# Kernel optimization log

Measured on AMD Instinct MI355X. Metric: run time of the kernel, lower is better.

## Reference

```python
import jax, jax.numpy as jnp
import numpy as np

H, DI, N, R, B, L, K = 1024, 2048, 16, 64, 1, 2048, 4


def setup_inputs() -> dict:
    key = jax.random.key(0)
    ks = jax.random.split(key, 12)
    s = 0.02
    x = jax.random.normal(ks[0], (B, L, H), dtype=jnp.float32)
    in_proj_w = jax.random.normal(ks[1], (2 * DI, H), dtype=jnp.float32) * s
    in_proj_b = jax.random.normal(ks[2], (2 * DI,), dtype=jnp.float32) * s
    conv_w = jax.random.normal(ks[3], (DI, 1, K), dtype=jnp.float32) * s
    conv_b = jax.random.normal(ks[4], (DI,), dtype=jnp.float32) * s
    x_proj_w = jax.random.normal(ks[5], (R + 2 * N, DI), dtype=jnp.float32) * s
    dt_init_std = R ** (-0.5)
    dt_proj_w = jax.random.uniform(ks[6], (DI, R), dtype=jnp.float32, minval=-dt_init_std, maxval=dt_init_std)
    dt = jnp.exp(jax.random.uniform(ks[7], (DI,), dtype=jnp.float32) * (np.log(0.1) - np.log(0.001)) + np.log(0.001))
    dt = jnp.clip(dt, 0.0001, None)
    dt_proj_b = dt + jnp.log(-jnp.expm1(-dt))
    A_log = jnp.log(jnp.broadcast_to(jnp.arange(1, N + 1, dtype=jnp.float32)[None, :], (DI, N)))
    D = jnp.ones((DI,), dtype=jnp.float32)
    out_proj_w = jax.random.normal(ks[8], (H, DI), dtype=jnp.float32) * s
    return {"x": x, "in_proj_w": in_proj_w, "in_proj_b": in_proj_b, "conv_w": conv_w,
            "conv_b": conv_b, "x_proj_w": x_proj_w, "dt_proj_w": dt_proj_w,
            "dt_proj_b": dt_proj_b, "A_log": A_log, "D": D, "out_proj_w": out_proj_w}


def _mamba_fwd(x, in_proj_w, in_proj_b, conv_w, conv_b, x_proj_w, dt_proj_w, dt_proj_b, A_log, D, out_proj_w):
    b, l, _ = x.shape
    x_and_res = x @ in_proj_w.T + in_proj_b               # [b, l, 2*DI]
    xc, res = jnp.split(x_and_res, 2, axis=-1)
    # causal depthwise conv1d (padding K-1 then truncate to l == left-pad only)
    xt = jnp.transpose(xc, (0, 2, 1))                     # [b, DI, l]
    conv = jax.lax.conv_general_dilated(
        xt, conv_w, window_strides=(1,), padding=[(K - 1, 0)],
        dimension_numbers=("NCH", "OIH", "NCH"), feature_group_count=DI)
    conv = conv + conv_b[None, :, None]
    xs = jnp.transpose(jax.nn.silu(conv), (0, 2, 1))      # [b, l, DI]
    # SSM
    A = -jnp.exp(A_log.astype(jnp.float32))               # [DI, N]
    x_dbl = xs @ x_proj_w.T                               # [b, l, R+2N]
    delta, Bm, Cm = jnp.split(x_dbl, [R, R + N], axis=-1)
    delta = jax.nn.softplus(delta @ dt_proj_w.T + dt_proj_b)   # [b, l, DI]
    deltaA = jnp.exp(delta[..., None] * A[None, None])         # [b, l, DI, N]
    deltaB_u = delta[..., None] * Bm[:, :, None, :] * xs[..., None]

    def comb(c1, c2):
        a1, u1 = c1
        a2, u2 = c2
        return a2 * a1, a2 * u1 + u2

    _, h = jax.lax.associative_scan(comb, (deltaA, deltaB_u), axis=1)
    y = jnp.einsum("bldn,bln->bld", h, Cm) + xs * D.astype(jnp.float32)
    y = y * jax.nn.silu(res)
    return y @ out_proj_w.T                               # [b, l, H]


def reference(x, in_proj_w, in_proj_b, conv_w, conv_b, x_proj_w, dt_proj_w, dt_proj_b, A_log, D, out_proj_w):
    return _mamba_fwd(x, in_proj_w, in_proj_b, conv_w, conv_b, x_proj_w,
                      dt_proj_w, dt_proj_b, A_log, D, out_proj_w)
```

## Files before the change

kernel.cpp:

```cpp
#include <hip/hip_runtime.h>
#include <hip/hip_bf16.h>
#include <math.h>

#define H_DIM 1024
#define DI    2048
#define NS    16
#define RR    64
#define LL    2048
#define NC    64
#define CL    32
#define KSPL  16

typedef __bf16 bf16x8 __attribute__((ext_vector_type(8)));
typedef __bf16 bf16x4 __attribute__((ext_vector_type(4)));
typedef float  f32x4  __attribute__((ext_vector_type(4)));

__device__ __forceinline__ float silu_f(float x)  { return x / (1.f + __expf(-x)); }
__device__ __forceinline__ float softplus_f(float x) {
    const float l = __logf(1.f + __expf(x));
    return x > 15.f ? x : l;
}

__device__ __forceinline__ void gload16(const void* g, void* l) {
    __builtin_amdgcn_global_load_lds(
        (const __attribute__((address_space(1))) void*)g,
        (__attribute__((address_space(3))) void*)l, 16, 0, 0);
}

__device__ __forceinline__ void f2b4(const float* __restrict__ in,
                                     __bf16* __restrict__ out)
{
    float4 v = *(const float4*)in;
    bf16x4 o;
    o[0] = (__bf16)v.x; o[1] = (__bf16)v.y; o[2] = (__bf16)v.z; o[3] = (__bf16)v.w;
    *(bf16x4*)out = o;
}

__device__ __forceinline__ void xcd_swz(int nx, int ny, int& bx, int& by)
{
    const int nwg = nx * ny;
    const int bid = by * nx + bx;
    const int cpx = nwg >> 3;
    const int s   = (bid & 7) * cpx + (bid >> 3);
    bx = s % nx;  by = s / nx;
}

#define SEG0 (LL * H_DIM)
#define SEG1 (2 * DI * H_DIM)
#define SEG2 (H_DIM * DI)
#define SEG3 (DI * RR)
#define SEG4 (128 * DI)
#define CUM0 SEG0
#define CUM1 (CUM0 + SEG1)
#define CUM2 (CUM1 + SEG2)
#define CUM3 (CUM2 + SEG3)
#define CUMT (CUM3 + SEG4)

__global__ __launch_bounds__(256) void convert_all_k(
    const float* __restrict__ x,    const float* __restrict__ in_w,
    const float* __restrict__ outw, const float* __restrict__ dtw,
    const float* __restrict__ xpw,
    __bf16* __restrict__ x_bf,    __bf16* __restrict__ inw_bf,
    __bf16* __restrict__ outw_bf, __bf16* __restrict__ dtw_bf,
    __bf16* __restrict__ xpw_pad)
{
    const int i = (blockIdx.x * 256 + threadIdx.x) * 4;
    if (i < CUM0) {
        f2b4(x + i, x_bf + i);
    } else if (i < CUM1) {
        const int o = i - CUM0;  f2b4(in_w + o, inw_bf + o);
    } else if (i < CUM2) {
        const int o = i - CUM1;  f2b4(outw + o, outw_bf + o);
    } else if (i < CUM3) {
        const int o = i - CUM2;  f2b4(dtw + o, dtw_bf + o);
    } else if (i < CUMT) {
        const int o = i - CUM3;
        const int row = o >> 11;
        if (row < 96) {
            f2b4(xpw + o, xpw_pad + o);
        } else {
            bf16x4 z; z[0] = z[1] = z[2] = z[3] = (__bf16)0.f;
            *(bf16x4*)&xpw_pad[o] = z;
        }
    }
}

__global__ __launch_bounds__(256) void reduce_xdbl_k(
    const float* __restrict__ part, float* __restrict__ xdbl,
    __bf16* __restrict__ xdbl_bf)
{
    const int idx = blockIdx.x * 256 + threadIdx.x;
    float s = 0.f;
    #pragma unroll
    for (int z = 0; z < KSPL; ++z) s += part[(size_t)z * (LL * 96) + idx];
    xdbl[idx] = s;
    xdbl_bf[idx] = (__bf16)s;
}

__global__ __launch_bounds__(256) void reduce_out_k(
    const float* __restrict__ part, float* __restrict__ out)
{
    const int i = (blockIdx.x * 256 + threadIdx.x) * 4;
    f32x4 a = *(const f32x4*)&part[i];
    f32x4 b = *(const f32x4*)&part[(size_t)LL * H_DIM + i];
    *(f32x4*)&out[i] = a + b;
}

#define WAIT_VM3()  asm volatile("s_waitcnt vmcnt(3)" ::: "memory")
#define WAIT_VM0()  asm volatile("s_waitcnt vmcnt(0)" ::: "memory")

__global__ __launch_bounds__(256) void gemm_inproj_k(
    const __bf16* __restrict__ A,
    const __bf16* __restrict__ W,
    const float* __restrict__ bias,
    __bf16* __restrict__ xc_bf,
    __bf16* __restrict__ res_bf)
{
    __shared__ __bf16 smA[3][64 * 32];
    __shared__ __bf16 smB[3][128 * 32];
    const int t    = threadIdx.x;
    const int lane = t & 63;
    int bx = blockIdx.x, by = blockIdx.y;
    xcd_swz(32, 32, bx, by);
    const int m0 = by * 64, n0 = bx * 128;
    const int wr = ((t >> 6) >> 1) * 32;
    const int wc = ((t >> 6) & 1) * 64;

    const int srow = t >> 2;
    const int skof = (t & 3) * 8;
    const int lds_base = (t >> 6) * 512;

    const int offA = (wr + (lane & 15)) * 32 + ((lane >> 4) * 8);
    const int offB = (wc + (lane & 15)) * 32 + ((lane >> 4) * 8);

    f32x4 acc[2][4] = {};

#define STAGE_IP(buf, k0)                                                          \
    do {                                                                           \
        gload16(A + (size_t)(m0 + srow)      * H_DIM + (k0) + skof, &smA[buf][lds_base]);        \
        gload16(W + (size_t)(n0 + srow)      * H_DIM + (k0) + skof, &smB[buf][lds_base]);        \
        gload16(W + (size_t)(n0 + 64 + srow) * H_DIM + (k0) + skof, &smB[buf][2048 + lds_base]); \
    } while (0)

    const int nk = H_DIM / 32;
    STAGE_IP(0, 0);
    STAGE_IP(1, 32);
    for (int ks = 0; ks < nk; ++ks) {
        if (ks + 1 < nk) WAIT_VM3(); else WAIT_VM0();
        __builtin_amdgcn_s_barrier();
        if (ks + 2 < nk) STAGE_IP((ks + 2) % 3, (ks + 2) * 32);
        const int cb = ks % 3;

        bf16x8 af[2], bfr[4];
        #pragma unroll
        for (int m = 0; m < 2; ++m) af[m]  = *(const bf16x8*)&smA[cb][offA + m * 512];
        #pragma unroll
        for (int n = 0; n < 4; ++n) bfr[n] = *(const bf16x8*)&smB[cb][offB + n * 512];
        #pragma unroll
        for (int m = 0; m < 2; ++m)
            #pragma unroll
            for (int n = 0; n < 4; ++n)
                acc[m][n] = __builtin_amdgcn_mfma_f32_16x16x32_bf16(
                    af[m], bfr[n], acc[m][n], 0, 0, 0);
    }
#undef STAGE_IP

    __bf16* outp = (n0 < DI) ? xc_bf : res_bf;
    const int ncol0 = (n0 < DI) ? n0 : n0 - DI;
    const int rbase = m0 + wr + ((lane >> 4) << 2);
    const int cbase = ncol0 + wc + (lane & 15);
    #pragma unroll
    for (int n = 0; n < 4; ++n) {
        const int col = cbase + n * 16;
        const float bv = bias[(n0 < DI ? 0 : DI) + col];
        #pragma unroll
        for (int m = 0; m < 2; ++m)
            #pragma unroll
            for (int j = 0; j < 4; ++j)
                outp[(size_t)(rbase + m * 16 + j) * DI + col] =
                    (__bf16)(acc[m][n][j] + bv);
    }
}

template<int BIAS, int ACT, int SPLITK, int SWZ>
__global__ __launch_bounds__(256) void gemm64_bf16_nt(
    const __bf16* __restrict__ A, int lda,
    const __bf16* __restrict__ W, int ldw,
    const float* __restrict__ bias,
    float* __restrict__ C, int ldc, int ncols, size_t pstride,
    int K)
{
    __shared__ __bf16 smA[3][64 * 32];
    __shared__ __bf16 smB[3][128 * 32];
    const int t    = threadIdx.x;
    const int lane = t & 63;
    int bx = blockIdx.x, by = blockIdx.y;
    if (SWZ) xcd_swz(gridDim.x, gridDim.y, bx, by);
    const int m0 = by * 64, n0 = bx * 128;
    const int wr = ((t >> 6) >> 1) * 32;
    const int wc = ((t >> 6) & 1) * 64;

    const int srow = t >> 2;
    const int skof = (t & 3) * 8;
    const int lds_base = (t >> 6) * 512;

    const int offA = (wr + (lane & 15)) * 32 + ((lane >> 4) * 8);
    const int offB = (wc + (lane & 15)) * 32 + ((lane >> 4) * 8);

    const int kseg  = K / SPLITK;
    const int kbase = (SPLITK > 1) ? blockIdx.z * kseg : 0;

    f32x4 acc[2][4] = {};

#define STAGE_64(buf, k0)                                                          \
    do {                                                                           \
        gload16(A + (size_t)(m0 + srow)      * lda + (k0) + skof, &smA[buf][lds_base]);        \
        gload16(W + (size_t)(n0 + srow)      * ldw + (k0) + skof, &smB[buf][lds_base]);        \
        gload16(W + (size_t)(n0 + 64 + srow) * ldw + (k0) + skof, &smB[buf][2048 + lds_base]); \
    } while (0)

    const int nk = kseg / 32;
    STAGE_64(0, kbase);
    if (nk > 1) STAGE_64(1, kbase + 32);
    for (int ks = 0; ks < nk; ++ks) {
        if (ks + 1 < nk) WAIT_VM3(); else WAIT_VM0();
        __builtin_amdgcn_s_barrier();
        if (ks + 2 < nk) STAGE_64((ks + 2) % 3, kbase + (ks + 2) * 32);
        const int cb = ks % 3;

        bf16x8 af[2], bfr[4];
        #pragma unroll
        for (int m = 0; m < 2; ++m) af[m]  = *(const bf16x8*)&smA[cb][offA + m * 512];
        #pragma unroll
        for (int n = 0; n < 4; ++n) bfr[n] = *(const bf16x8*)&smB[cb][offB + n * 512];
        #pragma unroll
        for (int m = 0; m < 2; ++m)
            #pragma unroll
            for (int n = 0; n < 4; ++n)
                acc[m][n] = __builtin_amdgcn_mfma_f32_16x16x32_bf16(
                    af[m], bfr[n], acc[m][n], 0, 0, 0);
    }
#undef STAGE_64

    float* Cp = C + ((SPLITK > 1) ? (size_t)blockIdx.z * pstride : 0);
    const int rbase = m0 + wr + ((lane >> 4) << 2);
    const int cbase = n0 + wc + (lane & 15);
    #pragma unroll
    for (int n = 0; n < 4; ++n) {
        const int col = cbase + n * 16;
        if (col >= ncols) continue;
        const float bv = BIAS ? bias[col] : 0.f;
        #pragma unroll
        for (int m = 0; m < 2; ++m) {
            #pragma unroll
            for (int j = 0; j < 4; ++j) {
                float v = acc[m][n][j] + bv;
                if (ACT == 1) v = softplus_f(v);
                Cp[(size_t)(rbase + m * 16 + j) * ldc + col] = v;
            }
        }
    }
}

__global__ __launch_bounds__(256) void conv_silu_k(
    const __bf16* __restrict__ xc, const float* __restrict__ cw,
    const float* __restrict__ cb, __bf16* __restrict__ xs_bf)
{
    const int idx = blockIdx.x * 256 + threadIdx.x;
    const int l  = idx >> 8;
    const int d0 = (idx & 255) * 8;

    float r0[8] = {}, r1[8] = {}, r2[8] = {}, r3[8];
    bf16x8 v;
    if (l >= 3) { v = *(const bf16x8*)&xc[(size_t)(l-3)*DI + d0];
                  #pragma unroll
                  for (int j = 0; j < 8; ++j) r0[j] = (float)v[j]; }
    if (l >= 2) { v = *(const bf16x8*)&xc[(size_t)(l-2)*DI + d0];
                  #pragma unroll
                  for (int j = 0; j < 8; ++j) r1[j] = (float)v[j]; }
    if (l >= 1) { v = *(const bf16x8*)&xc[(size_t)(l-1)*DI + d0];
                  #pragma unroll
                  for (int j = 0; j < 8; ++j) r2[j] = (float)v[j]; }
    v = *(const bf16x8*)&xc[(size_t)l*DI + d0];
    #pragma unroll
    for (int j = 0; j < 8; ++j) r3[j] = (float)v[j];

    bf16x8 o;
    #pragma unroll
    for (int j = 0; j < 8; ++j) {
        const int d = d0 + j;
        float4 w = *(const float4*)&cw[d * 4];
        float a = cb[d];
        a = fmaf(r0[j], w.x, a);
        a = fmaf(r1[j], w.y, a);
        a = fmaf(r2[j], w.z, a);
        a = fmaf(r3[j], w.w, a);
        o[j] = (__bf16)silu_f(a);
    }
    *(bf16x8*)&xs_bf[(size_t)l*DI + d0] = o;
}

__global__ __launch_bounds__(256) void scan1_k(
    const float* __restrict__ delta, const __bf16* __restrict__ xs,
    const float* __restrict__ A_log, const float* __restrict__ xdbl,
    float* __restrict__ P, float* __restrict__ S)
{
    const int d = blockIdx.x * 256 + threadIdx.x;
    const int c = blockIdx.y;
    float A[NS];
    #pragma unroll
    for (int n = 0; n < NS; ++n) A[n] = -__expf(A_log[d * NS + n]);
    float h[NS] = {};
    float ap[NS];
    #pragma unroll
    for (int n = 0; n < NS; ++n) ap[n] = 1.f;

    const int l0 = c * CL;
    for (int l = l0; l < l0 + CL; ++l) {
        const float dt = delta[(size_t)l * DI + d];
        const float u  = (float)xs[(size_t)l * DI + d];
        const float du = dt * u;
        #pragma unroll
        for (int n = 0; n < NS; ++n) {
            const float Bn = xdbl[(size_t)l * 96 + RR + n];
            const float dA = __expf(dt * A[n]);
            h[n]  = fmaf(dA, h[n], du * Bn);
            ap[n] *= dA;
        }
    }
    const size_t base = ((size_t)c * DI + d) * NS;
    #pragma unroll
    for (int n = 0; n < NS; ++n) { P[base + n] = ap[n]; S[base + n] = h[n]; }
}

__global__ __launch_bounds__(256) void scan2_k(
    const float* __restrict__ P, const float* __restrict__ S, float* __restrict__ Hp)
{
    const int idx = blockIdx.x * 256 + threadIdx.x;
    float h = 0.f;
    for (int c = 0; c < NC; ++c) {
        const size_t o = (size_t)c * DI * NS + idx;
        Hp[o] = h;
        h = fmaf(P[o], h, S[o]);
    }
}

__global__ __launch_bounds__(256) void scan3_k(
    const float* __restrict__ delta, const __bf16* __restrict__ xs,
    const float* __restrict__ A_log, const float* __restrict__ xdbl,
    const float* __restrict__ Hp, const __bf16* __restrict__ res_bf,
    const float* __restrict__ Dp, __bf16* __restrict__ y_bf)
{
    const int d = blockIdx.x * 256 + threadIdx.x;
    const int c = blockIdx.y;
    float A[NS];
    #pragma unroll
    for (int n = 0; n < NS; ++n) A[n] = -__expf(A_log[d * NS + n]);
    float h[NS];
    const size_t base = ((size_t)c * DI + d) * NS;
    #pragma unroll
    for (int n = 0; n < NS; ++n) h[n] = Hp[base + n];
    const float Dd = Dp[d];

    const int l0 = c * CL;
    for (int l = l0; l < l0 + CL; ++l) {
        const float dt = delta[(size_t)l * DI + d];
        const float u  = (float)xs[(size_t)l * DI + d];
        const float du = dt * u;
        float acc = 0.f;
        #pragma unroll
        for (int n = 0; n < NS; ++n) {
            const float Bn = xdbl[(size_t)l * 96 + RR + n];
            const float Cn = xdbl[(size_t)l * 96 + RR + NS + n];
            const float dA = __expf(dt * A[n]);
            h[n] = fmaf(dA, h[n], du * Bn);
            acc  = fmaf(h[n], Cn, acc);
        }
        float yv = fmaf(u, Dd, acc);
        const float r = (float)res_bf[(size_t)l * DI + d];
        yv *= silu_f(r);
        y_bf[(size_t)l * DI + d] = (__bf16)yv;
    }
}

extern "C" void kernel_launch(void* const* d_in, const int* in_sizes, int n_in,
                              void* d_out, int out_size, void* d_ws, size_t ws_size,
                              hipStream_t stream)
{
    const float* x        = (const float*)d_in[0];
    const float* in_w     = (const float*)d_in[1];
    const float* in_b     = (const float*)d_in[2];
    const float* conv_w   = (const float*)d_in[3];
    const float* conv_b   = (const float*)d_in[4];
    const float* xproj_w  = (const float*)d_in[5];
    const float* dtproj_w = (const float*)d_in[6];
    const float* dtproj_b = (const float*)d_in[7];
    const float* A_log    = (const float*)d_in[8];
    const float* Dp       = (const float*)d_in[9];
    const float* outw     = (const float*)d_in[10];
    float* out = (float*)d_out;

    float* ws    = (float*)d_ws;
    float* delta = ws;
    float* xdbl  = delta + (size_t)LL * DI;
    float* P     = xdbl  + (size_t)LL * 96;
    float* S     = P     + (size_t)NC * DI * NS;
    float* Hp    = S     + (size_t)NC * DI * NS;
    float* opart = Hp    + (size_t)NC * DI * NS;
    float* xpart = delta;
    __bf16* x_bf    = (__bf16*)(opart + (size_t)2 * LL * H_DIM);
    __bf16* inw_bf  = x_bf    + (size_t)LL * H_DIM;
    __bf16* outw_bf = inw_bf  + (size_t)2 * DI * H_DIM;
    __bf16* dtw_bf  = outw_bf + (size_t)H_DIM * DI;
    __bf16* xdbl_bf = dtw_bf  + (size_t)DI * RR;
    __bf16* y_bf    = xdbl_bf + (size_t)LL * 96;
    __bf16* xs_bf   = y_bf    + (size_t)LL * DI;
    __bf16* xc_bf   = xs_bf   + (size_t)LL * DI;
    __bf16* res_bf  = xc_bf   + (size_t)LL * DI;
    __bf16* xpw_pad = res_bf  + (size_t)LL * DI;

    const dim3 blk(256);

    convert_all_k<<<dim3(CUMT / 1024), blk, 0, stream>>>(
        x, in_w, outw, dtproj_w, xproj_w,
        x_bf, inw_bf, outw_bf, dtw_bf, xpw_pad);

    gemm_inproj_k<<<dim3((2*DI)/128, LL/64), blk, 0, stream>>>(
        x_bf, inw_bf, in_b, xc_bf, res_bf);

    conv_silu_k<<<dim3((LL*DI)/(8*256)), blk, 0, stream>>>(xc_bf, conv_w, conv_b, xs_bf);

    gemm64_bf16_nt<0,0,KSPL,0><<<dim3(1, LL/64, KSPL), blk, 0, stream>>>(
        xs_bf, DI, xpw_pad, DI, nullptr, xpart, 96, 96, (size_t)LL * 96, DI);
    reduce_xdbl_k<<<dim3((LL * 96) / 256), blk, 0, stream>>>(xpart, xdbl, xdbl_bf);

    gemm64_bf16_nt<1,1,1,1><<<dim3(DI/128, LL/64), blk, 0, stream>>>(
        xdbl_bf, 96, dtw_bf, RR, dtproj_b, delta, DI, DI, 0, RR);

    scan1_k<<<dim3(DI/256, NC), blk, 0, stream>>>(delta, xs_bf, A_log, xdbl, P, S);
    scan2_k<<<dim3((DI*NS)/256), blk, 0, stream>>>(P, S, Hp);
    scan3_k<<<dim3(DI/256, NC), blk, 0, stream>>>(delta, xs_bf, A_log, xdbl, Hp, res_bf, Dp, y_bf);

    gemm64_bf16_nt<0,0,2,1><<<dim3(H_DIM/128, LL/64, 2), blk, 0, stream>>>(
        y_bf, DI, outw_bf, DI, nullptr, opart, H_DIM, H_DIM, (size_t)LL * H_DIM, DI);
    reduce_out_k<<<dim3((LL * H_DIM) / 1024), blk, 0, stream>>>(opart, out);
}
```

Measured before the change: 243.7 us.

## Switch GEMMs to 32-row tiles and drop split-K on out_proj

Replaces the 64x128 triple-buffered GEMM with a 32x128 tile, double-buffered variant using __syncthreads between stages, with each wave owning a 32-column slice. The out_proj GEMM now runs without split-K and writes directly to the output, removing the partial buffer and the reduce kernel. The smaller M tile doubles the block count to keep occupancy up without split-K. In exchange, each block does half as much work per loaded B tile, and the loop drops from three buffers to two with a full barrier every step, which gives less load/compute overlap.

```diff
diff --git a/kernel.cpp b/kernel.cpp
--- a/kernel.cpp
+++ b/kernel.cpp
@@ -97,15 +97,6 @@
     xdbl_bf[idx] = (__bf16)s;
 }
 
-__global__ __launch_bounds__(256) void reduce_out_k(
-    const float* __restrict__ part, float* __restrict__ out)
-{
-    const int i = (blockIdx.x * 256 + threadIdx.x) * 4;
-    f32x4 a = *(const f32x4*)&part[i];
-    f32x4 b = *(const f32x4*)&part[(size_t)LL * H_DIM + i];
-    *(f32x4*)&out[i] = a + b;
-}
-
 #define WAIT_VM3()  asm volatile("s_waitcnt vmcnt(3)" ::: "memory")
 #define WAIT_VM0()  asm volatile("s_waitcnt vmcnt(0)" ::: "memory")
 
@@ -183,70 +174,70 @@
 }
 
 template<int BIAS, int ACT, int SPLITK, int SWZ>
-__global__ __launch_bounds__(256) void gemm64_bf16_nt(
+__global__ __launch_bounds__(256) void gemm32_bf16_nt(
     const __bf16* __restrict__ A, int lda,
     const __bf16* __restrict__ W, int ldw,
     const float* __restrict__ bias,
     float* __restrict__ C, int ldc, int ncols, size_t pstride,
     int K)
 {
-    __shared__ __bf16 smA[3][64 * 32];
-    __shared__ __bf16 smB[3][128 * 32];
+    __shared__ __bf16 smA[2][32 * 32];
+    __shared__ __bf16 smB[2][128 * 32];
     const int t    = threadIdx.x;
     const int lane = t & 63;
+    const int wv   = t >> 6;
     int bx = blockIdx.x, by = blockIdx.y;
     if (SWZ) xcd_swz(gridDim.x, gridDim.y, bx, by);
-    const int m0 = by * 64, n0 = bx * 128;
-    const int wr = ((t >> 6) >> 1) * 32;
-    const int wc = ((t >> 6) & 1) * 64;
+    const int m0 = by * 32, n0 = bx * 128;
 
     const int srow = t >> 2;
     const int skof = (t & 3) * 8;
-    const int lds_base = (t >> 6) * 512;
-
-    const int offA = (wr + (lane & 15)) * 32 + ((lane >> 4) * 8);
-    const int offB = (wc + (lane & 15)) * 32 + ((lane >> 4) * 8);
+    const int lds_base = wv * 512;
+
+    const int offA = (lane & 15) * 32 + ((lane >> 4) * 8);
+    const int offB = (wv * 32 + (lane & 15)) * 32 + ((lane >> 4) * 8);
 
     const int kseg  = K / SPLITK;
     const int kbase = (SPLITK > 1) ? blockIdx.z * kseg : 0;
-
-    f32x4 acc[2][4] = {};
-
-#define STAGE_64(buf, k0)                                                          \
+    const int kend  = kbase + kseg;
+
+    f32x4 acc[2][2] = {};
+
+#define STAGE_32(buf, k0)                                                          \
     do {                                                                           \
-        gload16(A + (size_t)(m0 + srow)      * lda + (k0) + skof, &smA[buf][lds_base]);        \
+        if (t < 128)                                                               \
+            gload16(A + (size_t)(m0 + srow)  * lda + (k0) + skof, &smA[buf][lds_base]);        \
         gload16(W + (size_t)(n0 + srow)      * ldw + (k0) + skof, &smB[buf][lds_base]);        \
         gload16(W + (size_t)(n0 + 64 + srow) * ldw + (k0) + skof, &smB[buf][2048 + lds_base]); \
     } while (0)
 
-    const int nk = kseg / 32;
-    STAGE_64(0, kbase);
-    if (nk > 1) STAGE_64(1, kbase + 32);
-    for (int ks = 0; ks < nk; ++ks) {
-        if (ks + 1 < nk) WAIT_VM3(); else WAIT_VM0();
-        __builtin_amdgcn_s_barrier();
-        if (ks + 2 < nk) STAGE_64((ks + 2) % 3, kbase + (ks + 2) * 32);
-        const int cb = ks % 3;
-
-        bf16x8 af[2], bfr[4];
-        #pragma unroll
-        for (int m = 0; m < 2; ++m) af[m]  = *(const bf16x8*)&smA[cb][offA + m * 512];
-        #pragma unroll
-        for (int n = 0; n < 4; ++n) bfr[n] = *(const bf16x8*)&smB[cb][offB + n * 512];
+    STAGE_32(0, kbase);
+    __syncthreads();
+    int cur = 0;
+    for (int k0 = kbase; k0 < kend; k0 += 32) {
+        if (k0 + 32 < kend) STAGE_32(cur ^ 1, k0 + 32);
+
+        bf16x8 af[2], bfr[2];
+        #pragma unroll
+        for (int m = 0; m < 2; ++m) af[m]  = *(const bf16x8*)&smA[cur][offA + m * 512];
+        #pragma unroll
+        for (int n = 0; n < 2; ++n) bfr[n] = *(const bf16x8*)&smB[cur][offB + n * 512];
         #pragma unroll
         for (int m = 0; m < 2; ++m)
             #pragma unroll
-            for (int n = 0; n < 4; ++n)
+            for (int n = 0; n < 2; ++n)
                 acc[m][n] = __builtin_amdgcn_mfma_f32_16x16x32_bf16(
                     af[m], bfr[n], acc[m][n], 0, 0, 0);
-    }
-#undef STAGE_64
+        __syncthreads();
+        cur ^= 1;
+    }
+#undef STAGE_32
 
     float* Cp = C + ((SPLITK > 1) ? (size_t)blockIdx.z * pstride : 0);
-    const int rbase = m0 + wr + ((lane >> 4) << 2);
-    const int cbase = n0 + wc + (lane & 15);
-    #pragma unroll
-    for (int n = 0; n < 4; ++n) {
+    const int rbase = m0 + ((lane >> 4) << 2);
+    const int cbase = n0 + wv * 32 + (lane & 15);
+    #pragma unroll
+    for (int n = 0; n < 2; ++n) {
         const int col = cbase + n * 16;
         if (col >= ncols) continue;
         const float bv = BIAS ? bias[col] : 0.f;
@@ -406,9 +397,8 @@
     float* P     = xdbl  + (size_t)LL * 96;
     float* S     = P     + (size_t)NC * DI * NS;
     float* Hp    = S     + (size_t)NC * DI * NS;
-    float* opart = Hp    + (size_t)NC * DI * NS;
     float* xpart = delta;
-    __bf16* x_bf    = (__bf16*)(opart + (size_t)2 * LL * H_DIM);
+    __bf16* x_bf    = (__bf16*)(Hp + (size_t)NC * DI * NS);
     __bf16* inw_bf  = x_bf    + (size_t)LL * H_DIM;
     __bf16* outw_bf = inw_bf  + (size_t)2 * DI * H_DIM;
     __bf16* dtw_bf  = outw_bf + (size_t)H_DIM * DI;
@@ -430,18 +420,17 @@
 
     conv_silu_k<<<dim3((LL*DI)/(8*256)), blk, 0, stream>>>(xc_bf, conv_w, conv_b, xs_bf);
 
-    gemm64_bf16_nt<0,0,KSPL,0><<<dim3(1, LL/64, KSPL), blk, 0, stream>>>(
+    gemm32_bf16_nt<0,0,KSPL,0><<<dim3(1, LL/32, KSPL), blk, 0, stream>>>(
         xs_bf, DI, xpw_pad, DI, nullptr, xpart, 96, 96, (size_t)LL * 96, DI);
     reduce_xdbl_k<<<dim3((LL * 96) / 256), blk, 0, stream>>>(xpart, xdbl, xdbl_bf);
 
-    gemm64_bf16_nt<1,1,1,1><<<dim3(DI/128, LL/64), blk, 0, stream>>>(
+    gemm32_bf16_nt<1,1,1,1><<<dim3(DI/128, LL/32), blk, 0, stream>>>(
         xdbl_bf, 96, dtw_bf, RR, dtproj_b, delta, DI, DI, 0, RR);
 
     scan1_k<<<dim3(DI/256, NC), blk, 0, stream>>>(delta, xs_bf, A_log, xdbl, P, S);
     scan2_k<<<dim3((DI*NS)/256), blk, 0, stream>>>(P, S, Hp);
     scan3_k<<<dim3(DI/256, NC), blk, 0, stream>>>(delta, xs_bf, A_log, xdbl, Hp, res_bf, Dp, y_bf);
 
-    gemm64_bf16_nt<0,0,2,1><<<dim3(H_DIM/128, LL/64, 2), blk, 0, stream>>>(
-        y_bf, DI, outw_bf, DI, nullptr, opart, H_DIM, H_DIM, (size_t)LL * H_DIM, DI);
-    reduce_out_k<<<dim3((LL * H_DIM) / 1024), blk, 0, stream>>>(opart, out);
-}
+    gemm32_bf16_nt<0,0,1,1><<<dim3(H_DIM/128, LL/32), blk, 0, stream>>>(
+        y_bf, DI, outw_bf, DI, nullptr, out, H_DIM, H_DIM, 0, DI);
+}
```

After: 245.5 us. No clear change (+0.7%).
